# Performance work log

Measured on AMD Instinct MI355X. Metric: run time of the kernel, lower is better.

The kernel has to match this reference:

```python
import jax, jax.numpy as jnp
import numpy as np

N_HEADS = 16
DIM = 1024
DH = DIM // N_HEADS  # 64
B, S = 4, 2048


def setup_inputs() -> dict:
    key = jax.random.key(0)
    k1, k2, k3, k4 = jax.random.split(key, 4)
    x = jax.random.normal(k1, (B, S, DIM), dtype=jnp.float32)
    src_mask = jax.random.uniform(k2, (B, S)) < 0.1
    # torch nn.Linear weights: y = x @ W.T
    W_qkv = jax.random.normal(k3, (3 * DIM, DIM), dtype=jnp.float32) * (DIM ** -0.5)
    W_o = jax.random.normal(k4, (DIM, DIM), dtype=jnp.float32) * (DIM ** -0.5)
    return {"x": x, "src_mask": src_mask, "W_qkv": W_qkv, "W_o": W_o}


def reference(x, src_mask, W_qkv, W_o):
    b, s, _ = x.shape
    qkv = x @ W_qkv.T  # [b, s, 3*DIM]
    # rearrange 'b s (n_h d) -> ... ' BEFORE chunk(3): head h owns a contiguous
    # 3*DH slice, which is then split into q,k,v of DH each.
    qkv = qkv.reshape(b, s, N_HEADS, 3 * DH)
    q, k, v = jnp.split(qkv, 3, axis=-1)  # each [b, s, h, dh]
    logits = jnp.einsum('bqhd,bkhd->bhqk', q, k) * (DH ** -0.5)
    logits = jnp.where(src_mask[:, None, None, :], -jnp.inf, logits)
    attn = jax.nn.softmax(logits, axis=-1)  # dropout=0.0 -> identity
    out = jnp.einsum('bhqk,bkhd->bqhd', attn, v).reshape(b, s, DIM)
    return out @ W_o.T
```

## Files before the change

kernel.cpp:

```cpp
#include <hip/hip_runtime.h>
#include <hip/hip_bf16.h>
#include <stdint.h>


typedef unsigned short u16;
typedef __attribute__((ext_vector_type(8)))  short    bf16x8;
typedef __attribute__((ext_vector_type(8)))  unsigned short u16x8;
typedef __attribute__((ext_vector_type(4)))  unsigned short u16x4;
typedef __attribute__((ext_vector_type(4)))  float    f32x4;
typedef __attribute__((ext_vector_type(16))) float    f32x16;
typedef __attribute__((ext_vector_type(4)))  unsigned int u32x4;
typedef __attribute__((ext_vector_type(4)))  int      i32x4;

#define DEVI __device__ __forceinline__

DEVI u16 f2bf(float f) {
    union { float f; uint32_t u; } v; v.f = f;
    uint32_t r = v.u + 0x7fffu + ((v.u >> 16) & 1u);
    return (u16)(r >> 16);
}

#define GLDS(gp, lp) __builtin_amdgcn_global_load_lds( \
    (const __attribute__((address_space(1))) void*)(gp), \
    (__attribute__((address_space(3))) void*)(lp), 16, 0, 0)

#define MFMA16(a, b, c) __builtin_amdgcn_mfma_f32_16x16x32_bf16(a, b, c, 0, 0, 0)
#define MFMA32(a, b, c) __builtin_amdgcn_mfma_f32_32x32x16_bf16(a, b, c, 0, 0, 0)

#define CVTPK(d, lo, hi) asm("v_cvt_pk_bf16_f32 %0, %1, %2" : "=v"(d) : "v"(lo), "v"(hi))
#define PLSWAP(a, b) asm("v_permlane32_swap_b32 %0, %1" : "+v"(a), "+v"(b))

#define QSCALE 0.1803368801111204f

__global__ __launch_bounds__(256) void cvt_f32_bf16(const float* __restrict__ in,
                                                    u16* __restrict__ out, int n4) {
    int i = blockIdx.x * 256 + threadIdx.x;
    if (i >= n4) return;
    f32x4 v = *(const f32x4*)(in + (size_t)i * 4);
    u16x4 o;
#pragma unroll
    for (int j = 0; j < 4; j++) o[j] = f2bf(v[j]);
    *(u16x4*)(out + (size_t)i * 4) = o;
}

template <int MODE>
__global__ __launch_bounds__(256) void gemm_bt(const u16* __restrict__ A,
                                               const u16* __restrict__ B,
                                               void* __restrict__ C,
                                               int M, int N, int K) {
    __shared__ u16 As[128 * 32];
    __shared__ u16 Bs[128 * 32];
    const int lane = threadIdx.x & 63;
    const int wave = threadIdx.x >> 6;
    const int mT = blockIdx.y * 128;
    const int nT = blockIdx.x * 128;

    const int srow = wave * 16 + (lane >> 2);
    const int skc  = (lane & 3) * 8;
    const u16* gA = A + (size_t)(mT + srow) * K + skc;
    const u16* gB = B + (size_t)(nT + srow) * K + skc;
    u16* lA = As + wave * 512;
    u16* lB = Bs + wave * 512;

    f32x4 acc[4][4];
#pragma unroll
    for (int m = 0; m < 4; m++)
#pragma unroll
        for (int n = 0; n < 4; n++) acc[m][n] = f32x4{0.f, 0.f, 0.f, 0.f};

    const int wm = (wave >> 1) * 64, wn = (wave & 1) * 64;
    const int fr = lane & 15, fg = lane >> 4;

    for (int kt = 0; kt < K; kt += 32) {
        GLDS(gA + kt, lA);
        GLDS(gA + kt + (size_t)64 * K, lA + 2048);
        GLDS(gB + kt, lB);
        GLDS(gB + kt + (size_t)64 * K, lB + 2048);
        __syncthreads();
        bf16x8 af[4], bg[4];
#pragma unroll
        for (int m = 0; m < 4; m++)
            af[m] = *(const bf16x8*)(As + (wm + m * 16 + fr) * 32 + fg * 8);
#pragma unroll
        for (int n = 0; n < 4; n++)
            bg[n] = *(const bf16x8*)(Bs + (wn + n * 16 + fr) * 32 + fg * 8);
#pragma unroll
        for (int m = 0; m < 4; m++)
#pragma unroll
            for (int n = 0; n < 4; n++)
                acc[m][n] = MFMA16(af[m], bg[n], acc[m][n]);
        __syncthreads();
    }

    float qs[4];
#pragma unroll
    for (int n = 0; n < 4; n++) {
        if (MODE == 2) {
            int col = nT + wn + n * 16 + fr;
            qs[n] = ((col % 192) < 64) ? QSCALE : 1.0f;
        } else qs[n] = 1.0f;
    }
#pragma unroll
    for (int m = 0; m < 4; m++)
#pragma unroll
        for (int r = 0; r < 4; r++) {
            int row = mT + wm + m * 16 + fg * 4 + r;
#pragma unroll
            for (int n = 0; n < 4; n++) {
                int col = nT + wn + n * 16 + fr;
                if (MODE == 0) ((float*)C)[(size_t)row * N + col] = acc[m][n][r];
                else           ((u16*)C)[(size_t)row * N + col] = f2bf(acc[m][n][r] * qs[n]);
            }
        }
}

__global__ __launch_bounds__(256) void transpose_v(const u16* __restrict__ qkv,
                                                   const int* __restrict__ mask,
                                                   u16* __restrict__ vT) {
    __shared__ u16 tile[64][72];
    const int tid = threadIdx.x;
    const int b = blockIdx.z, h = blockIdx.y;
    const int s0 = blockIdx.x * 64;
    const int r = tid >> 3, c = tid & 7;

#pragma unroll
    for (int p = 0; p < 2; p++) {
        int s = p * 32 + r;
        u16x8 v = *(const u16x8*)(qkv + (size_t)(b * 2048 + s0 + s) * 3072
                                  + h * 192 + 128 + c * 8);
        if (mask[b * 2048 + s0 + s]) v = u16x8{0, 0, 0, 0, 0, 0, 0, 0};
#pragma unroll
        for (int j = 0; j < 8; j++) tile[c * 8 + j][s] = v[j];
    }
    __syncthreads();
#pragma unroll
    for (int p = 0; p < 2; p++) {
        int d = p * 32 + r;
        u16x8 v = *(const u16x8*)(&tile[d][c * 8]);
        *(u16x8*)(vT + ((size_t)((b * 16 + h) * 64 + d)) * 2048 + s0 + c * 8) = v;
    }
}

__global__ __launch_bounds__(256, 3) void attn_kernel(const u16* __restrict__ qkv,
                                                      const u16* __restrict__ vT,
                                                      const int* __restrict__ mask,
                                                      u16* __restrict__ ctx) {
    __shared__ u16 Kl[2][4096];
    __shared__ u16 Vl[2][4096];
    __shared__ u16 keeps[2048];

    const int lane = threadIdx.x & 63;
    const int wave = threadIdx.x >> 6;
    const int hl = lane >> 5;
    const int l31 = lane & 31;

    const int fid = blockIdx.x + 16 * blockIdx.y + 256 * blockIdx.z;
    const int swz = (fid & 7) * 128 + (fid >> 3);
    const int b = swz >> 8, h = (swz >> 4) & 15;
    const int qT = (swz & 15) * 128;

    {
        const i32x4* mp = (const i32x4*)(mask + b * 2048) + threadIdx.x * 2;
        i32x4 m0 = mp[0], m1 = mp[1];
        u16x8 kp;
#pragma unroll
        for (int j = 0; j < 4; j++) {
            kp[j]     = m0[j] ? (u16)0 : (u16)0x3F80;
            kp[4 + j] = m1[j] ? (u16)0 : (u16)0x3F80;
        }
        *(u16x8*)(keeps + threadIdx.x * 8) = kp;
    }

    const u16* qrow = qkv + (size_t)(b * 2048 + qT + wave * 32 + l31) * 3072 + h * 192;
    bf16x8 aq[4];
#pragma unroll
    for (int c = 0; c < 4; c++) aq[c] = *(const bf16x8*)(qrow + c * 16 + hl * 8);

    const int r0 = wave * 16 + (lane >> 3);
    const int j0 = (lane & 7) ^ (r0 & 7);
    const u16* kg = qkv + (size_t)(b * 2048 + r0) * 3072 + h * 192 + 64 + j0 * 8;
    const u16* vg = vT + ((size_t)((b * 16 + h) * 64) + r0) * 2048 + j0 * 8;

#define STAGE(tt, bb) do { \
        const u16* kgp = kg + (size_t)(tt) * (64 * 3072); \
        const u16* vgp = vg + (size_t)(tt) * 64; \
        u16* lK = Kl[bb] + wave * 1024; \
        u16* lV = Vl[bb] + wave * 1024; \
        GLDS(kgp, lK); GLDS(kgp + (size_t)8 * 3072, lK + 512); \
        GLDS(vgp, lV); GLDS(vgp + (size_t)8 * 2048, lV + 512); \
    } while (0)

    STAGE(0, 0);

    f32x16 so0, so1, lacc;
#pragma unroll
    for (int i = 0; i < 16; i++) { so0[i] = 0.f; so1[i] = 0.f; lacc[i] = 0.f; }

    const int swc = l31 & 7;

    __syncthreads();

    int buf = 0;
    for (int t = 0; t < 32; ++t) {
        if (t < 31) STAGE(t + 1, buf ^ 1);
        const u16* kc = Kl[buf];
        const u16* vc = Vl[buf];
        const int kb = t * 64;

        f32x16 s0, s1;
#pragma unroll
        for (int i = 0; i < 16; i++) { s0[i] = 0.f; s1[i] = 0.f; }
#pragma unroll
        for (int c = 0; c < 4; c++) {
            const int ch = ((c * 2 + hl) ^ swc) * 8;
            bf16x8 ka0 = *(const bf16x8*)(kc + l31 * 64 + ch);
            bf16x8 ka1 = *(const bf16x8*)(kc + (32 + l31) * 64 + ch);
            s0 = MFMA32(ka0, aq[c], s0);
            s1 = MFMA32(ka1, aq[c], s1);
        }

#pragma unroll
        for (int i = 0; i < 16; i++) { s0[i] = exp2f(s0[i]); s1[i] = exp2f(s1[i]); }

        uint32_t u0, u1, u2, u3, u4, u5, u6, u7;
        bf16x8 pa0, pa1, pa2, pa3;
        CVTPK(u0, s0[0], s0[1]);  CVTPK(u1, s0[2], s0[3]);
        CVTPK(u2, s0[4], s0[5]);  CVTPK(u3, s0[6], s0[7]);
        CVTPK(u4, s0[8], s0[9]);  CVTPK(u5, s0[10], s0[11]);
        CVTPK(u6, s0[12], s0[13]); CVTPK(u7, s0[14], s0[15]);
        PLSWAP(u0, u2); PLSWAP(u1, u3); PLSWAP(u4, u6); PLSWAP(u5, u7);
        pa0 = __builtin_bit_cast(bf16x8, u32x4{u0, u1, u2, u3});
        pa1 = __builtin_bit_cast(bf16x8, u32x4{u4, u5, u6, u7});
        CVTPK(u0, s1[0], s1[1]);  CVTPK(u1, s1[2], s1[3]);
        CVTPK(u2, s1[4], s1[5]);  CVTPK(u3, s1[6], s1[7]);
        CVTPK(u4, s1[8], s1[9]);  CVTPK(u5, s1[10], s1[11]);
        CVTPK(u6, s1[12], s1[13]); CVTPK(u7, s1[14], s1[15]);
        PLSWAP(u0, u2); PLSWAP(u1, u3); PLSWAP(u4, u6); PLSWAP(u5, u7);
        pa2 = __builtin_bit_cast(bf16x8, u32x4{u0, u1, u2, u3});
        pa3 = __builtin_bit_cast(bf16x8, u32x4{u4, u5, u6, u7});

#pragma unroll
        for (int c = 0; c < 4; c++) {
            const bf16x8 pa = (c == 0) ? pa0 : (c == 1) ? pa1 : (c == 2) ? pa2 : pa3;
            const int ch = ((c * 2 + hl) ^ swc) * 8;
            bf16x8 bv0 = *(const bf16x8*)(vc + l31 * 64 + ch);
            bf16x8 bv1 = *(const bf16x8*)(vc + (32 + l31) * 64 + ch);
            bf16x8 kp  = *(const bf16x8*)(keeps + kb + c * 16 + hl * 8);
            so0 = MFMA32(pa, bv0, so0);
            so1 = MFMA32(pa, bv1, so1);
            lacc = MFMA32(pa, kp, lacc);
        }

        __syncthreads();
        buf ^= 1;
    }

#pragma unroll
    for (int r = 0; r < 16; r++) {
        const int q = qT + wave * 32 + (r & 3) + 8 * (r >> 2) + 4 * hl;
        const float inv = 1.0f / lacc[r];
        u16* crow = ctx + (size_t)(b * 2048 + q) * 1024 + h * 64 + l31;
        crow[0]  = f2bf(so0[r] * inv);
        crow[32] = f2bf(so1[r] * inv);
    }
#undef STAGE
}

extern "C" void kernel_launch(void* const* d_in, const int* in_sizes, int n_in,
                              void* d_out, int out_size, void* d_ws, size_t ws_size,
                              hipStream_t stream) {
    const float* x    = (const float*)d_in[0];
    const int*   mask = (const int*)d_in[1];
    const float* Wqkv = (const float*)d_in[2];
    const float* Wo   = (const float*)d_in[3];
    float* out = (float*)d_out;

    char* ws = (char*)d_ws;
    u16* xb    = (u16*)(ws);
    u16* wqkvb = (u16*)(ws + 16777216);
    u16* wob   = (u16*)(ws + 23068672);
    u16* qkvb  = (u16*)(ws + 25165824);
    u16* ctxb  = (u16*)(ws + 75497472);
    u16* vTb   = xb;

    cvt_f32_bf16<<<8192, 256, 0, stream>>>(x, xb, 8388608 / 4);
    cvt_f32_bf16<<<3072, 256, 0, stream>>>(Wqkv, wqkvb, 3145728 / 4);
    cvt_f32_bf16<<<1024, 256, 0, stream>>>(Wo, wob, 1048576 / 4);

    gemm_bt<2><<<dim3(24, 64), 256, 0, stream>>>(xb, wqkvb, qkvb, 8192, 3072, 1024);
    transpose_v<<<dim3(32, 16, 4), 256, 0, stream>>>(qkvb, mask, vTb);
    attn_kernel<<<dim3(16, 16, 4), 256, 0, stream>>>(qkvb, vTb, mask, ctxb);
    gemm_bt<0><<<dim3(8, 64), 256, 0, stream>>>(ctxb, wob, out, 8192, 1024, 1024);
}
```

Before: 233.8 us.

## Process two KV tiles per barrier with quad-buffered LDS, polynomial exp2 and setprio

Restructures the attention loop to stage and compute two 64-key tiles per iteration using four LDS buffers, halving the number of block barriers. exp2f is replaced by a bit-manipulation polynomial exp2, and s_setprio is raised around the MFMA sections. Launch bounds drop from 3 to 2 blocks per CU because of the doubled shared memory. The changes aim to cut barrier and transcendental overhead, at the cost of lower occupancy and slightly different exp precision.

```diff
diff --git a/kernel.cpp b/kernel.cpp
--- a/kernel.cpp
+++ b/kernel.cpp
@@ -18,6 +18,16 @@
     union { float f; uint32_t u; } v; v.f = f;
     uint32_t r = v.u + 0x7fffu + ((v.u >> 16) & 1u);
     return (u16)(r >> 16);
+}
+
+DEVI float fexp2(float x) {
+    float t = x + 12582912.0f;
+    float f = x - (t - 12582912.0f);
+    float p = 1.0f + f * (0.69314718f + f * (0.24022650f
+                   + f * (0.05550411f + f * 0.00961813f)));
+    uint32_t pb = __builtin_bit_cast(uint32_t, p)
+                + (__builtin_bit_cast(uint32_t, t) << 23);
+    return __builtin_bit_cast(float, pb);
 }
 
 #define GLDS(gp, lp) __builtin_amdgcn_global_load_lds( \
@@ -141,12 +151,12 @@
     }
 }
 
-__global__ __launch_bounds__(256, 3) void attn_kernel(const u16* __restrict__ qkv,
+__global__ __launch_bounds__(256, 2) void attn_kernel(const u16* __restrict__ qkv,
                                                       const u16* __restrict__ vT,
                                                       const int* __restrict__ mask,
                                                       u16* __restrict__ ctx) {
-    __shared__ u16 Kl[2][4096];
-    __shared__ u16 Vl[2][4096];
+    __shared__ u16 Kl[4][4096];
+    __shared__ u16 Vl[4][4096];
     __shared__ u16 keeps[2048];
 
     const int lane = threadIdx.x & 63;
@@ -181,79 +191,99 @@
     const u16* kg = qkv + (size_t)(b * 2048 + r0) * 3072 + h * 192 + 64 + j0 * 8;
     const u16* vg = vT + ((size_t)((b * 16 + h) * 64) + r0) * 2048 + j0 * 8;
 
-#define STAGE(tt, bb) do { \
-        const u16* kgp = kg + (size_t)(tt) * (64 * 3072); \
-        const u16* vgp = vg + (size_t)(tt) * 64; \
-        u16* lK = Kl[bb] + wave * 1024; \
-        u16* lV = Vl[bb] + wave * 1024; \
-        GLDS(kgp, lK); GLDS(kgp + (size_t)8 * 3072, lK + 512); \
-        GLDS(vgp, lV); GLDS(vgp + (size_t)8 * 2048, lV + 512); \
+    u16* const ksd[4] = { Kl[0] + wave * 1024, Kl[1] + wave * 1024,
+                          Kl[2] + wave * 1024, Kl[3] + wave * 1024 };
+    u16* const vsd[4] = { Vl[0] + wave * 1024, Vl[1] + wave * 1024,
+                          Vl[2] + wave * 1024, Vl[3] + wave * 1024 };
+
+#define STAGEP(gk, gv, bi) do { \
+        GLDS((gk), ksd[bi]); GLDS((gk) + (size_t)8 * 3072, ksd[bi] + 512); \
+        GLDS((gv), vsd[bi]); GLDS((gv) + (size_t)8 * 2048, vsd[bi] + 512); \
     } while (0)
 
-    STAGE(0, 0);
+    STAGEP(kg, vg, 0);
+    STAGEP(kg + (size_t)64 * 3072, vg + 64, 1);
+
+    const u16* kgn = kg + (size_t)128 * 3072;
+    const u16* vgn = vg + 128;
+    const u16* kpb = keeps + hl * 8;
 
     f32x16 so0, so1, lacc;
 #pragma unroll
     for (int i = 0; i < 16; i++) { so0[i] = 0.f; so1[i] = 0.f; lacc[i] = 0.f; }
+    f32x16 Z16;
+#pragma unroll
+    for (int i = 0; i < 16; i++) Z16[i] = 0.f;
 
     const int swc = l31 & 7;
 
     __syncthreads();
 
-    int buf = 0;
-    for (int t = 0; t < 32; ++t) {
-        if (t < 31) STAGE(t + 1, buf ^ 1);
-        const u16* kc = Kl[buf];
-        const u16* vc = Vl[buf];
-        const int kb = t * 64;
-
-        f32x16 s0, s1;
-#pragma unroll
-        for (int i = 0; i < 16; i++) { s0[i] = 0.f; s1[i] = 0.f; }
-#pragma unroll
-        for (int c = 0; c < 4; c++) {
-            const int ch = ((c * 2 + hl) ^ swc) * 8;
-            bf16x8 ka0 = *(const bf16x8*)(kc + l31 * 64 + ch);
-            bf16x8 ka1 = *(const bf16x8*)(kc + (32 + l31) * 64 + ch);
-            s0 = MFMA32(ka0, aq[c], s0);
-            s1 = MFMA32(ka1, aq[c], s1);
+#define COMPUTE(kc, vc, kpbase) do { \
+        f32x16 s0, s1; \
+        __builtin_amdgcn_s_setprio(1); \
+        _Pragma("unroll") \
+        for (int c = 0; c < 4; c++) { \
+            const int ch = ((c * 2 + hl) ^ swc) * 8; \
+            bf16x8 ka0 = *(const bf16x8*)((kc) + l31 * 64 + ch); \
+            bf16x8 ka1 = *(const bf16x8*)((kc) + (32 + l31) * 64 + ch); \
+            if (c == 0) { s0 = MFMA32(ka0, aq[0], Z16); s1 = MFMA32(ka1, aq[0], Z16); } \
+            else        { s0 = MFMA32(ka0, aq[c], s0);  s1 = MFMA32(ka1, aq[c], s1); } \
+        } \
+        __builtin_amdgcn_s_setprio(0); \
+        _Pragma("unroll") \
+        for (int i = 0; i < 16; i++) { s0[i] = fexp2(s0[i]); s1[i] = fexp2(s1[i]); } \
+        uint32_t u0, u1, u2, u3, u4, u5, u6, u7; \
+        bf16x8 pa0, pa1, pa2, pa3; \
+        CVTPK(u0, s0[0], s0[1]);   CVTPK(u1, s0[2], s0[3]); \
+        CVTPK(u2, s0[4], s0[5]);   CVTPK(u3, s0[6], s0[7]); \
+        CVTPK(u4, s0[8], s0[9]);   CVTPK(u5, s0[10], s0[11]); \
+        CVTPK(u6, s0[12], s0[13]); CVTPK(u7, s0[14], s0[15]); \
+        PLSWAP(u0, u2); PLSWAP(u1, u3); PLSWAP(u4, u6); PLSWAP(u5, u7); \
+        pa0 = __builtin_bit_cast(bf16x8, u32x4{u0, u1, u2, u3}); \
+        pa1 = __builtin_bit_cast(bf16x8, u32x4{u4, u5, u6, u7}); \
+        CVTPK(u0, s1[0], s1[1]);   CVTPK(u1, s1[2], s1[3]); \
+        CVTPK(u2, s1[4], s1[5]);   CVTPK(u3, s1[6], s1[7]); \
+        CVTPK(u4, s1[8], s1[9]);   CVTPK(u5, s1[10], s1[11]); \
+        CVTPK(u6, s1[12], s1[13]); CVTPK(u7, s1[14], s1[15]); \
+        PLSWAP(u0, u2); PLSWAP(u1, u3); PLSWAP(u4, u6); PLSWAP(u5, u7); \
+        pa2 = __builtin_bit_cast(bf16x8, u32x4{u0, u1, u2, u3}); \
+        pa3 = __builtin_bit_cast(bf16x8, u32x4{u4, u5, u6, u7}); \
+        __builtin_amdgcn_s_setprio(1); \
+        _Pragma("unroll") \
+        for (int c = 0; c < 4; c++) { \
+            const bf16x8 pa = (c == 0) ? pa0 : (c == 1) ? pa1 : (c == 2) ? pa2 : pa3; \
+            const int ch = ((c * 2 + hl) ^ swc) * 8; \
+            bf16x8 bv0 = *(const bf16x8*)((vc) + l31 * 64 + ch); \
+            bf16x8 bv1 = *(const bf16x8*)((vc) + (32 + l31) * 64 + ch); \
+            bf16x8 kp  = *(const bf16x8*)((kpbase) + c * 16); \
+            so0 = MFMA32(pa, bv0, so0); \
+            so1 = MFMA32(pa, bv1, so1); \
+            lacc = MFMA32(pa, kp, lacc); \
+        } \
+        __builtin_amdgcn_s_setprio(0); \
+    } while (0)
+
+    for (int it = 0; it < 16; ++it) {
+        const int p2 = (it & 1) * 2;
+        if (it < 15) {
+            const int q2 = p2 ^ 2;
+            STAGEP(kgn, vgn, q2);
+            STAGEP(kgn + (size_t)64 * 3072, vgn + 64, q2 + 1);
+            kgn += (size_t)128 * 3072;
+            vgn += 128;
         }
-
-#pragma unroll
-        for (int i = 0; i < 16; i++) { s0[i] = exp2f(s0[i]); s1[i] = exp2f(s1[i]); }
-
-        uint32_t u0, u1, u2, u3, u4, u5, u6, u7;
-        bf16x8 pa0, pa1, pa2, pa3;
-        CVTPK(u0, s0[0], s0[1]);  CVTPK(u1, s0[2], s0[3]);
-        CVTPK(u2, s0[4], s0[5]);  CVTPK(u3, s0[6], s0[7]);
-        CVTPK(u4, s0[8], s0[9]);  CVTPK(u5, s0[10], s0[11]);
-        CVTPK(u6, s0[12], s0[13]); CVTPK(u7, s0[14], s0[15]);
-        PLSWAP(u0, u2); PLSWAP(u1, u3); PLSWAP(u4, u6); PLSWAP(u5, u7);
-        pa0 = __builtin_bit_cast(bf16x8, u32x4{u0, u1, u2, u3});
-        pa1 = __builtin_bit_cast(bf16x8, u32x4{u4, u5, u6, u7});
-        CVTPK(u0, s1[0], s1[1]);  CVTPK(u1, s1[2], s1[3]);
-        CVTPK(u2, s1[4], s1[5]);  CVTPK(u3, s1[6], s1[7]);
-        CVTPK(u4, s1[8], s1[9]);  CVTPK(u5, s1[10], s1[11]);
-        CVTPK(u6, s1[12], s1[13]); CVTPK(u7, s1[14], s1[15]);
-        PLSWAP(u0, u2); PLSWAP(u1, u3); PLSWAP(u4, u6); PLSWAP(u5, u7);
-        pa2 = __builtin_bit_cast(bf16x8, u32x4{u0, u1, u2, u3});
-        pa3 = __builtin_bit_cast(bf16x8, u32x4{u4, u5, u6, u7});
-
-#pragma unroll
-        for (int c = 0; c < 4; c++) {
-            const bf16x8 pa = (c == 0) ? pa0 : (c == 1) ? pa1 : (c == 2) ? pa2 : pa3;
-            const int ch = ((c * 2 + hl) ^ swc) * 8;
-            bf16x8 bv0 = *(const bf16x8*)(vc + l31 * 64 + ch);
-            bf16x8 bv1 = *(const bf16x8*)(vc + (32 + l31) * 64 + ch);
-            bf16x8 kp  = *(const bf16x8*)(keeps + kb + c * 16 + hl * 8);
-            so0 = MFMA32(pa, bv0, so0);
-            so1 = MFMA32(pa, bv1, so1);
-            lacc = MFMA32(pa, kp, lacc);
-        }
-
+        const u16* kcA = Kl[p2];
+        const u16* vcA = Vl[p2];
+        COMPUTE(kcA, vcA, kpb);
+        const u16* kcB = Kl[p2 + 1];
+        const u16* vcB = Vl[p2 + 1];
+        COMPUTE(kcB, vcB, kpb + 64);
+        kpb += 128;
         __syncthreads();
-        buf ^= 1;
-    }
+    }
+#undef COMPUTE
+#undef STAGEP
 
 #pragma unroll
     for (int r = 0; r < 16; r++) {
@@ -263,7 +293,6 @@
         crow[0]  = f2bf(so0[r] * inv);
         crow[32] = f2bf(so1[r] * inv);
     }
-#undef STAGE
 }
 
 extern "C" void kernel_launch(void* const* d_in, const int* in_sizes, int n_in,
```

New measurement: 242.4 us. 3.7% more time.
